# Kernel tuning notes

Hardware: AMD Instinct MI355X
Metric: run time of the kernel (lower is better)

The kernel has to match this reference:

```python
import jax, jax.numpy as jnp
import numpy as np
import math

NA, D, DA = 8, 512, 64
BSZ, THW = 4, 1024
EPS = 1e-5


def setup_inputs() -> dict:
    key = jax.random.key(0)
    ks = jax.random.split(key, 8)
    x = jax.random.normal(ks[0], (BSZ, THW, D), dtype=jnp.float32)
    B = jax.random.normal(ks[1], (NA, BSZ, THW, THW), dtype=jnp.float32)
    M = jax.random.randint(ks[2], (THW, THW), 0, 2, dtype=jnp.int32)
    # xavier-normal-ish params
    def xavier(k, shape, fan_in, fan_out):
        std = math.sqrt(2.0 / (fan_in + fan_out))
        return jax.random.normal(k, shape, dtype=jnp.float32) * std
    w_q = xavier(ks[3], (NA, D, DA), D, DA)
    w_k = xavier(ks[4], (NA, D, DA), D, DA)
    w_v = xavier(ks[5], (NA, D, DA), D, DA)
    w_proj = xavier(ks[6], (D, NA * DA), NA * DA, D)  # nn.Linear weight [out, in]
    gamma = jnp.ones((D,), dtype=jnp.float32)
    beta = jnp.zeros((D,), dtype=jnp.float32)
    return {"x": x, "B": B, "M": M, "gamma": gamma, "beta": beta,
            "w_q": w_q, "w_k": w_k, "w_v": w_v, "w_proj": w_proj}


def reference(x, B, M, gamma, beta, w_q, w_k, w_v, w_proj):
    b, thw, d = x.shape
    na, _, da = w_q.shape
    # pre-LayerNorm (residual is un-normalized x)
    mu = jnp.mean(x, axis=-1, keepdims=True)
    var = jnp.mean(jnp.square(x - mu), axis=-1, keepdims=True)
    xn = (x - mu) / jnp.sqrt(var + EPS) * gamma + beta  # [b, thw, d]
    # per-head QKV via shared projections: [na, b, thw, da]
    q = jnp.einsum('btd,hde->hbte', xn, w_q)
    k = jnp.einsum('btd,hde->hbte', xn, w_k)
    v = jnp.einsum('btd,hde->hbte', xn, w_v)
    temper = math.sqrt(da)
    attn = jnp.einsum('hbqe,hbke->hbqk', q, k) / temper + B  # [na, b, thw, thw]
    attn = jnp.where(M.astype(bool), jnp.float32(-10000.0), attn)
    p = jax.nn.softmax(attn, axis=-1)
    out = jnp.einsum('hbqk,hbke->hbqe', p, v)  # [na, b, thw, da]
    # concat heads on feature dim: [b, thw, na*da]
    out = out.transpose(1, 2, 0, 3).reshape(b, thw, na * da)
    out = out @ w_proj.T  # [b, thw, d]
    return out + x
```

## Files before the change

### kernel.cpp

```cpp
#include <hip/hip_runtime.h>

typedef __attribute__((ext_vector_type(4))) float f32x4;
typedef __attribute__((ext_vector_type(8))) short bf16x8;

#define AS1 __attribute__((address_space(1)))
#define AS3 __attribute__((address_space(3)))

static __device__ __forceinline__ void gl_lds16(const void* g, void* l) {
  __builtin_amdgcn_global_load_lds((const AS1 unsigned int*)g, (AS3 unsigned int*)l, 16, 0, 0);
}

static __device__ __forceinline__ unsigned short f2bf(float f) {
  union { float f; unsigned u; } v; v.f = f;
  unsigned r = v.u + 0x7FFFu + ((v.u >> 16) & 1u);
  return (unsigned short)(r >> 16);
}

__global__ __launch_bounds__(256) void prep_kernel(
    const float* __restrict__ wq, const float* __restrict__ wk,
    const float* __restrict__ wv, const float* __restrict__ wp,
    const int* __restrict__ M,
    unsigned short* __restrict__ Wt, unsigned short* __restrict__ Wp,
    unsigned* __restrict__ Mbits) {
  const int blk = blockIdx.x, tid = threadIdx.x;
  if (blk < 192) {
    __shared__ unsigned short t[64][72];
    const int which = blk >> 6, rem = blk & 63;
    const int h = rem >> 3, dt = rem & 7, d0 = dt * 64;
    const float* w = (which == 0) ? wq : ((which == 1) ? wk : wv);
    const float scale = (which == 0) ? 0.125f : 1.0f;
    const int r = tid >> 2, c4 = tid & 3;
    const float* src = w + h * 32768 + (d0 + r) * 64 + c4 * 16;
#pragma unroll
    for (int i = 0; i < 4; ++i) {
      float4 v = *(const float4*)(src + i * 4);
      t[c4 * 16 + i * 4 + 0][r] = f2bf(v.x * scale);
      t[c4 * 16 + i * 4 + 1][r] = f2bf(v.y * scale);
      t[c4 * 16 + i * 4 + 2][r] = f2bf(v.z * scale);
      t[c4 * 16 + i * 4 + 3][r] = f2bf(v.w * scale);
    }
    __syncthreads();
    const int e = tid >> 2;
    const int n = which * 512 + h * 64 + e;
    unsigned short* dst = Wt + (size_t)n * 512 + d0 + c4 * 16;
#pragma unroll
    for (int i = 0; i < 2; ++i) {
      bf16x8 o;
#pragma unroll
      for (int k = 0; k < 8; ++k) o[k] = (short)t[e][c4 * 16 + i * 8 + k];
      *(bf16x8*)(dst + i * 8) = o;
    }
  } else if (blk < 320) {
    const int base = ((blk - 192) * 256 + tid) * 8;
    float4 a = *(const float4*)(wp + base);
    float4 c = *(const float4*)(wp + base + 4);
    bf16x8 o;
    o[0] = (short)f2bf(a.x); o[1] = (short)f2bf(a.y);
    o[2] = (short)f2bf(a.z); o[3] = (short)f2bf(a.w);
    o[4] = (short)f2bf(c.x); o[5] = (short)f2bf(c.y);
    o[6] = (short)f2bf(c.z); o[7] = (short)f2bf(c.w);
    *(bf16x8*)(Wp + base) = o;
  } else {
    const int wi = (blk - 320) * 256 + tid;
    const int* row = M + wi * 32;
    unsigned bits = 0;
#pragma unroll
    for (int i = 0; i < 8; ++i) {
      int4 v = *(const int4*)(row + i * 4);
      bits |= (v.x != 0 ? 1u : 0u) << (i * 4 + 0);
      bits |= (v.y != 0 ? 1u : 0u) << (i * 4 + 1);
      bits |= (v.z != 0 ? 1u : 0u) << (i * 4 + 2);
      bits |= (v.w != 0 ? 1u : 0u) << (i * 4 + 3);
    }
    Mbits[wi] = bits;
  }
}


__global__ __launch_bounds__(256) void ln_kernel(
    const float* __restrict__ x, const float* __restrict__ gamma,
    const float* __restrict__ beta, unsigned short* __restrict__ xn) {
  const int wave = threadIdx.x >> 6, lane = threadIdx.x & 63;
  const int m = blockIdx.x * 4 + wave;
  const float* row = x + (size_t)m * 512;
  float4 a = *(const float4*)(row + lane * 8);
  float4 c = *(const float4*)(row + lane * 8 + 4);
  float s = a.x + a.y + a.z + a.w + c.x + c.y + c.z + c.w;
  float q = a.x * a.x + a.y * a.y + a.z * a.z + a.w * a.w +
            c.x * c.x + c.y * c.y + c.z * c.z + c.w * c.w;
#pragma unroll
  for (int off = 1; off < 64; off <<= 1) {
    s += __shfl_xor(s, off);
    q += __shfl_xor(q, off);
  }
  float mean = s * 0.001953125f;
  float var = q * 0.001953125f - mean * mean;
  float rstd = rsqrtf(var + 1e-5f);
  float4 g0 = *(const float4*)(gamma + lane * 8);
  float4 g1 = *(const float4*)(gamma + lane * 8 + 4);
  float4 b0 = *(const float4*)(beta + lane * 8);
  float4 b1 = *(const float4*)(beta + lane * 8 + 4);
  bf16x8 o;
  o[0] = (short)f2bf((a.x - mean) * rstd * g0.x + b0.x);
  o[1] = (short)f2bf((a.y - mean) * rstd * g0.y + b0.y);
  o[2] = (short)f2bf((a.z - mean) * rstd * g0.z + b0.z);
  o[3] = (short)f2bf((a.w - mean) * rstd * g0.w + b0.w);
  o[4] = (short)f2bf((c.x - mean) * rstd * g1.x + b1.x);
  o[5] = (short)f2bf((c.y - mean) * rstd * g1.y + b1.y);
  o[6] = (short)f2bf((c.z - mean) * rstd * g1.z + b1.z);
  o[7] = (short)f2bf((c.w - mean) * rstd * g1.w + b1.w);
  *(bf16x8*)(xn + (size_t)m * 512 + lane * 8) = o;
}

__global__ __launch_bounds__(256) void gemm_qkv(
    const unsigned short* __restrict__ A, const unsigned short* __restrict__ Bt,
    unsigned short* __restrict__ qout, unsigned short* __restrict__ kout,
    unsigned short* __restrict__ vout) {
  __shared__ __align__(16) unsigned short As[128 * 64];
  __shared__ __align__(16) unsigned short Bs[128 * 64];
  const int bx = blockIdx.x & 31, by = blockIdx.x >> 5;
  const int mbase = bx * 128, nbase = by * 128;
  const int tid = threadIdx.x;
  const int lane = tid & 63, wave = tid >> 6;
  const int lr = lane & 15, lg = lane >> 4;
  const int wm = wave >> 1, wn = wave & 1;
  f32x4 acc[4][4] = {};
  for (int kb = 0; kb < 8; ++kb) {
    const int kbase = kb * 64;
#pragma unroll
    for (int i = 0; i < 4; ++i) {
      int chunk = i * 256 + tid;
      int r = chunk >> 3, kc = chunk & 7;
      gl_lds16(A + (size_t)(mbase + r) * 512 + kbase + kc * 8, &As[chunk * 8]);
    }
#pragma unroll
    for (int i = 0; i < 4; ++i) {
      int chunk = i * 256 + tid;
      int r = chunk >> 3, kc = chunk & 7;
      gl_lds16(Bt + (size_t)(nbase + r) * 512 + kbase + kc * 8, &Bs[chunk * 8]);
    }
    __syncthreads();
#pragma unroll
    for (int ks = 0; ks < 2; ++ks) {
      bf16x8 af[4], bfr[4];
#pragma unroll
      for (int mi = 0; mi < 4; ++mi)
        af[mi] = *(const bf16x8*)&As[(wm * 64 + mi * 16 + lr) * 64 + ks * 32 + lg * 8];
#pragma unroll
      for (int ni = 0; ni < 4; ++ni)
        bfr[ni] = *(const bf16x8*)&Bs[(wn * 64 + ni * 16 + lr) * 64 + ks * 32 + lg * 8];
#pragma unroll
      for (int mi = 0; mi < 4; ++mi)
#pragma unroll
        for (int ni = 0; ni < 4; ++ni)
          acc[mi][ni] = __builtin_amdgcn_mfma_f32_16x16x32_bf16(af[mi], bfr[ni], acc[mi][ni], 0, 0, 0);
    }
    __syncthreads();
  }
#pragma unroll
  for (int ni = 0; ni < 4; ++ni) {
    const int n0 = nbase + wn * 64 + ni * 16;
    const int which = n0 >> 9, h = (n0 >> 6) & 7;
    const int e0 = (n0 & 63) + lr;
    unsigned short* dst = (which == 0) ? qout : ((which == 1) ? kout : vout);
    dst += (size_t)h * 262144 + e0;
#pragma unroll
    for (int mi = 0; mi < 4; ++mi) {
      const int m0 = mbase + wm * 64 + mi * 16 + lg * 4;
#pragma unroll
      for (int j = 0; j < 4; ++j) dst[(size_t)(m0 + j) * 64] = f2bf(acc[mi][ni][j]);
    }
  }
}

__global__ __launch_bounds__(256) void transpose_v(
    const unsigned short* __restrict__ vb, unsigned short* __restrict__ vt) {
  __shared__ unsigned short t[64][72];
  const int h = blockIdx.x >> 6, mt = blockIdx.x & 63;
  const unsigned short* src = vb + (size_t)h * 262144 + (size_t)mt * 64 * 64;
  const int tid = threadIdx.x;
#pragma unroll
  for (int i = 0; i < 2; ++i) {
    int c = tid + 256 * i;
    int r = c >> 3, c8 = c & 7;
    bf16x8 v = *(const bf16x8*)(src + r * 64 + c8 * 8);
#pragma unroll
    for (int k = 0; k < 8; ++k) t[c8 * 8 + k][r] = (unsigned short)v[k];
  }
  __syncthreads();
#pragma unroll
  for (int i = 0; i < 2; ++i) {
    int c = tid + 256 * i;
    int er = c >> 3, mc = c & 7;
    bf16x8 o;
#pragma unroll
    for (int k = 0; k < 8; ++k) o[k] = (short)t[er][mc * 8 + k];
    *(bf16x8*)(vt + (size_t)h * 262144 + (size_t)er * 4096 + mt * 64 + mc * 8) = o;
  }
}

__global__ __launch_bounds__(256, 2) void attn_kernel(
    const unsigned short* __restrict__ qb, const unsigned short* __restrict__ kbuf,
    const unsigned short* __restrict__ vt, const float* __restrict__ Bb,
    const unsigned* __restrict__ Mb, unsigned short* __restrict__ attno) {
  __shared__ __align__(16) unsigned short P[4][16 * 132];
  const int g = blockIdx.x;
  const int xcd = g & 7, slot = g >> 3;
  const int hb = xcd + 8 * (slot >> 4);
  const int qt = slot & 15;
  const int h = hb >> 2, b = hb & 3;
  const int lane = threadIdx.x & 63, wave = threadIdx.x >> 6;
  const int lr = lane & 15, lg = lane >> 4;
  const unsigned short* qh = qb + (size_t)h * 262144 + (size_t)b * 65536;
  const unsigned short* kh = kbuf + (size_t)h * 262144 + (size_t)b * 65536;
  const unsigned short* vh = vt + (size_t)h * 262144 + b * 1024;
  const int qa = qt * 64 + wave * 16 + lr;
  const bf16x8 qf0 = *(const bf16x8*)(qh + (size_t)qa * 64 + lg * 8);
  const bf16x8 qf1 = *(const bf16x8*)(qh + (size_t)qa * 64 + lg * 8 + 32);
  const int qc = qt * 64 + wave * 16 + lg * 4;
  const float* Bp = Bb + (size_t)hb * 1048576;
  float mrun[4] = {-1e30f, -1e30f, -1e30f, -1e30f};
  float lrun[4] = {0.f, 0.f, 0.f, 0.f};
  f32x4 of[4] = {};
  unsigned short* pw = &P[wave][0];
  for (int kv = 0; kv < 8; ++kv) {
    const int kvb = kv * 128;
    float bv[8][4];
    unsigned mwd[4][4];
#pragma unroll
    for (int j = 0; j < 4; ++j) {
      const float* brow = Bp + (size_t)(qc + j) * 1024 + kvb + lr;
#pragma unroll
      for (int f = 0; f < 8; ++f) bv[f][j] = brow[f * 16];
      uint4 mw = *(const uint4*)(Mb + (qc + j) * 32 + kv * 4);
      mwd[j][0] = mw.x; mwd[j][1] = mw.y; mwd[j][2] = mw.z; mwd[j][3] = mw.w;
    }
    bf16x8 kf0[8], kf1[8];
#pragma unroll
    for (int f = 0; f < 8; ++f) {
      const unsigned short* kp = kh + (size_t)(kvb + f * 16 + lr) * 64 + lg * 8;
      kf0[f] = *(const bf16x8*)kp;
      kf1[f] = *(const bf16x8*)(kp + 32);
    }
    f32x4 s[8];
#pragma unroll
    for (int f = 0; f < 8; ++f) {
      f32x4 c = {};
      c = __builtin_amdgcn_mfma_f32_16x16x32_bf16(qf0, kf0[f], c, 0, 0, 0);
      c = __builtin_amdgcn_mfma_f32_16x16x32_bf16(qf1, kf1[f], c, 0, 0, 0);
      s[f] = c;
    }
    float scl[4];
#pragma unroll
    for (int j = 0; j < 4; ++j) {
      float mm = -1e30f;
#pragma unroll
      for (int f = 0; f < 8; ++f) {
        float sv = s[f][j] + bv[f][j];
        if ((mwd[j][f >> 1] >> ((f & 1) * 16 + lr)) & 1u) sv = -10000.f;
        s[f][j] = sv;
        mm = fmaxf(mm, sv);
      }
      mm = fmaxf(mm, __shfl_xor(mm, 1));
      mm = fmaxf(mm, __shfl_xor(mm, 2));
      mm = fmaxf(mm, __shfl_xor(mm, 4));
      mm = fmaxf(mm, __shfl_xor(mm, 8));
      float mn = fmaxf(mrun[j], mm);
      scl[j] = __expf(mrun[j] - mn);
      mrun[j] = mn;
      float ps = 0.f;
#pragma unroll
      for (int f = 0; f < 8; ++f) {
        float p = __expf(s[f][j] - mn);
        s[f][j] = p;
        ps += p;
      }
      ps += __shfl_xor(ps, 1);
      ps += __shfl_xor(ps, 2);
      ps += __shfl_xor(ps, 4);
      ps += __shfl_xor(ps, 8);
      lrun[j] = lrun[j] * scl[j] + ps;
    }
#pragma unroll
    for (int e = 0; e < 4; ++e) {
      of[e][0] *= scl[0]; of[e][1] *= scl[1]; of[e][2] *= scl[2]; of[e][3] *= scl[3];
    }
#pragma unroll
    for (int f = 0; f < 8; ++f)
#pragma unroll
      for (int j = 0; j < 4; ++j)
        pw[(lg * 4 + j) * 132 + f * 16 + lr] = f2bf(s[f][j]);
    bf16x8 pa[4];
#pragma unroll
    for (int ks = 0; ks < 4; ++ks)
      pa[ks] = *(const bf16x8*)&pw[lr * 132 + ks * 32 + lg * 8];
    bf16x8 vf[4][4];
#pragma unroll
    for (int e = 0; e < 4; ++e) {
      const unsigned short* vp = vh + (size_t)(e * 16 + lr) * 4096 + kvb + lg * 8;
#pragma unroll
      for (int ks = 0; ks < 4; ++ks) vf[e][ks] = *(const bf16x8*)(vp + ks * 32);
    }
#pragma unroll
    for (int e = 0; e < 4; ++e)
#pragma unroll
      for (int ks = 0; ks < 4; ++ks)
        of[e] = __builtin_amdgcn_mfma_f32_16x16x32_bf16(pa[ks], vf[e][ks], of[e], 0, 0, 0);
  }
#pragma unroll
  for (int e = 0; e < 4; ++e)
#pragma unroll
    for (int j = 0; j < 4; ++j) {
      int m = b * 1024 + qc + j;
      attno[(size_t)h * 262144 + (size_t)m * 64 + e * 16 + lr] = f2bf(of[e][j] / lrun[j]);
    }
}

__global__ __launch_bounds__(256) void gemm_proj(
    const unsigned short* __restrict__ attno, const unsigned short* __restrict__ Wp,
    const float* __restrict__ x, float* __restrict__ out) {
  __shared__ __align__(16) unsigned short As[128 * 64];
  __shared__ __align__(16) unsigned short Bs[64 * 64];
  const int bx = blockIdx.x & 31, by = blockIdx.x >> 5;
  const int mbase = bx * 128, nbase = by * 64;
  const int tid = threadIdx.x;
  const int lane = tid & 63, wave = tid >> 6;
  const int lr = lane & 15, lg = lane >> 4;
  const int wm = wave >> 1, wn = wave & 1;
  f32x4 acc[4][2] = {};
  for (int kb = 0; kb < 8; ++kb) {
#pragma unroll
    for (int i = 0; i < 4; ++i) {
      int chunk = i * 256 + tid;
      int r = chunk >> 3, kc = chunk & 7;
      gl_lds16(attno + (size_t)kb * 262144 + (size_t)(mbase + r) * 64 + kc * 8, &As[chunk * 8]);
    }
#pragma unroll
    for (int i = 0; i < 2; ++i) {
      int chunk = i * 256 + tid;
      int r = chunk >> 3, kc = chunk & 7;
      gl_lds16(Wp + (size_t)(nbase + r) * 512 + kb * 64 + kc * 8, &Bs[chunk * 8]);
    }
    __syncthreads();
#pragma unroll
    for (int ks = 0; ks < 2; ++ks) {
      bf16x8 af[4], bfr[2];
#pragma unroll
      for (int mi = 0; mi < 4; ++mi)
        af[mi] = *(const bf16x8*)&As[(wm * 64 + mi * 16 + lr) * 64 + ks * 32 + lg * 8];
#pragma unroll
      for (int ni = 0; ni < 2; ++ni)
        bfr[ni] = *(const bf16x8*)&Bs[(wn * 32 + ni * 16 + lr) * 64 + ks * 32 + lg * 8];
#pragma unroll
      for (int mi = 0; mi < 4; ++mi)
#pragma unroll
        for (int ni = 0; ni < 2; ++ni)
          acc[mi][ni] = __builtin_amdgcn_mfma_f32_16x16x32_bf16(af[mi], bfr[ni], acc[mi][ni], 0, 0, 0);
    }
    __syncthreads();
  }
#pragma unroll
  for (int ni = 0; ni < 2; ++ni) {
    const int n = nbase + wn * 32 + ni * 16 + lr;
#pragma unroll
    for (int mi = 0; mi < 4; ++mi) {
      const int m0 = mbase + wm * 64 + mi * 16 + lg * 4;
#pragma unroll
      for (int j = 0; j < 4; ++j) {
        size_t idx = (size_t)(m0 + j) * 512 + n;
        out[idx] = acc[mi][ni][j] + x[idx];
      }
    }
  }
}

extern "C" void kernel_launch(void* const* d_in, const int* in_sizes, int n_in,
                              void* d_out, int out_size, void* d_ws, size_t ws_size,
                              hipStream_t stream) {
  const float* x = (const float*)d_in[0];
  const float* B = (const float*)d_in[1];
  const int* M = (const int*)d_in[2];
  const float* gamma = (const float*)d_in[3];
  const float* beta = (const float*)d_in[4];
  const float* wq = (const float*)d_in[5];
  const float* wk = (const float*)d_in[6];
  const float* wv = (const float*)d_in[7];
  const float* wp = (const float*)d_in[8];
  float* out = (float*)d_out;

  char* ws = (char*)d_ws;
  size_t o = 0;
  auto alloc = [&](size_t bytes) {
    void* p = ws + o;
    o += (bytes + 255) & ~(size_t)255;
    return p;
  };
  unsigned short* xn    = (unsigned short*)alloc(4096ull * 512 * 2);
  unsigned short* Wt    = (unsigned short*)alloc(1536ull * 512 * 2);
  unsigned short* Wp    = (unsigned short*)alloc(512ull * 512 * 2);
  unsigned*       Mb    = (unsigned*)alloc(1024ull * 32 * 4);
  unsigned short* qb    = (unsigned short*)alloc(8ull * 4096 * 64 * 2);
  unsigned short* kb    = (unsigned short*)alloc(8ull * 4096 * 64 * 2);
  unsigned short* vb    = (unsigned short*)alloc(8ull * 4096 * 64 * 2);
  unsigned short* vt    = (unsigned short*)alloc(8ull * 64 * 4096 * 2);
  unsigned short* attno = (unsigned short*)alloc(8ull * 4096 * 64 * 2);
  (void)ws_size; (void)in_sizes; (void)n_in; (void)out_size;

  hipLaunchKernelGGL(prep_kernel, dim3(448), dim3(256), 0, stream,
                     wq, wk, wv, wp, M, Wt, Wp, Mb);
  hipLaunchKernelGGL(ln_kernel, dim3(1024), dim3(256), 0, stream, x, gamma, beta, xn);
  hipLaunchKernelGGL(gemm_qkv, dim3(384), dim3(256), 0, stream, xn, Wt, qb, kb, vb);
  hipLaunchKernelGGL(transpose_v, dim3(512), dim3(256), 0, stream, vb, vt);
  hipLaunchKernelGGL(attn_kernel, dim3(512), dim3(256), 0, stream, qb, kb, vt, B, Mb, attno);
  hipLaunchKernelGGL(gemm_proj, dim3(256), dim3(256), 0, stream, attno, Wp, x, out);
}
```

Baseline: 293.5 us.

## Split attention over KV into four partitions with merge kernel; fuse LN into prep

The attention kernel becomes single-wave blocks, each handling 16 queries over one quarter of the key range. Each block writes unnormalized partial outputs plus running max and sum in fp32, and a new merge kernel combines the four partitions and writes bf16 output. This raises the grid from 512 to 8192 waves-blocks to improve latency hiding and occupancy on the memory-bound bias stream. The cost is extra fp32 partial traffic and one more launch. LayerNorm is also folded into the prep kernel to save a launch.

```diff
diff --git a/kernel.cpp b/kernel.cpp
--- a/kernel.cpp
+++ b/kernel.cpp
@@ -16,13 +16,47 @@
   return (unsigned short)(r >> 16);
 }
 
-__global__ __launch_bounds__(256) void prep_kernel(
+__global__ __launch_bounds__(256) void prepln_kernel(
     const float* __restrict__ wq, const float* __restrict__ wk,
     const float* __restrict__ wv, const float* __restrict__ wp,
-    const int* __restrict__ M,
+    const int* __restrict__ M, const float* __restrict__ x,
+    const float* __restrict__ gamma, const float* __restrict__ beta,
     unsigned short* __restrict__ Wt, unsigned short* __restrict__ Wp,
-    unsigned* __restrict__ Mbits) {
+    unsigned* __restrict__ Mbits, unsigned short* __restrict__ xn) {
   const int blk = blockIdx.x, tid = threadIdx.x;
+  if (blk >= 448) {
+    const int wave = tid >> 6, lane = tid & 63;
+    const int m = (blk - 448) * 4 + wave;
+    const float* row = x + (size_t)m * 512;
+    float4 a = *(const float4*)(row + lane * 8);
+    float4 c = *(const float4*)(row + lane * 8 + 4);
+    float s = a.x + a.y + a.z + a.w + c.x + c.y + c.z + c.w;
+    float q = a.x * a.x + a.y * a.y + a.z * a.z + a.w * a.w +
+              c.x * c.x + c.y * c.y + c.z * c.z + c.w * c.w;
+#pragma unroll
+    for (int off = 1; off < 64; off <<= 1) {
+      s += __shfl_xor(s, off);
+      q += __shfl_xor(q, off);
+    }
+    float mean = s * 0.001953125f;
+    float var = q * 0.001953125f - mean * mean;
+    float rstd = rsqrtf(var + 1e-5f);
+    float4 g0 = *(const float4*)(gamma + lane * 8);
+    float4 g1 = *(const float4*)(gamma + lane * 8 + 4);
+    float4 b0 = *(const float4*)(beta + lane * 8);
+    float4 b1 = *(const float4*)(beta + lane * 8 + 4);
+    bf16x8 o;
+    o[0] = (short)f2bf((a.x - mean) * rstd * g0.x + b0.x);
+    o[1] = (short)f2bf((a.y - mean) * rstd * g0.y + b0.y);
+    o[2] = (short)f2bf((a.z - mean) * rstd * g0.z + b0.z);
+    o[3] = (short)f2bf((a.w - mean) * rstd * g0.w + b0.w);
+    o[4] = (short)f2bf((c.x - mean) * rstd * g1.x + b1.x);
+    o[5] = (short)f2bf((c.y - mean) * rstd * g1.y + b1.y);
+    o[6] = (short)f2bf((c.z - mean) * rstd * g1.z + b1.z);
+    o[7] = (short)f2bf((c.w - mean) * rstd * g1.w + b1.w);
+    *(bf16x8*)(xn + (size_t)m * 512 + lane * 8) = o;
+    return;
+  }
   if (blk < 192) {
     __shared__ unsigned short t[64][72];
     const int which = blk >> 6, rem = blk & 63;
@@ -74,42 +108,6 @@
     }
     Mbits[wi] = bits;
   }
-}
-
-
-__global__ __launch_bounds__(256) void ln_kernel(
-    const float* __restrict__ x, const float* __restrict__ gamma,
-    const float* __restrict__ beta, unsigned short* __restrict__ xn) {
-  const int wave = threadIdx.x >> 6, lane = threadIdx.x & 63;
-  const int m = blockIdx.x * 4 + wave;
-  const float* row = x + (size_t)m * 512;
-  float4 a = *(const float4*)(row + lane * 8);
-  float4 c = *(const float4*)(row + lane * 8 + 4);
-  float s = a.x + a.y + a.z + a.w + c.x + c.y + c.z + c.w;
-  float q = a.x * a.x + a.y * a.y + a.z * a.z + a.w * a.w +
-            c.x * c.x + c.y * c.y + c.z * c.z + c.w * c.w;
-#pragma unroll
-  for (int off = 1; off < 64; off <<= 1) {
-    s += __shfl_xor(s, off);
-    q += __shfl_xor(q, off);
-  }
-  float mean = s * 0.001953125f;
-  float var = q * 0.001953125f - mean * mean;
-  float rstd = rsqrtf(var + 1e-5f);
-  float4 g0 = *(const float4*)(gamma + lane * 8);
-  float4 g1 = *(const float4*)(gamma + lane * 8 + 4);
-  float4 b0 = *(const float4*)(beta + lane * 8);
-  float4 b1 = *(const float4*)(beta + lane * 8 + 4);
-  bf16x8 o;
-  o[0] = (short)f2bf((a.x - mean) * rstd * g0.x + b0.x);
-  o[1] = (short)f2bf((a.y - mean) * rstd * g0.y + b0.y);
-  o[2] = (short)f2bf((a.z - mean) * rstd * g0.z + b0.z);
-  o[3] = (short)f2bf((a.w - mean) * rstd * g0.w + b0.w);
-  o[4] = (short)f2bf((c.x - mean) * rstd * g1.x + b1.x);
-  o[5] = (short)f2bf((c.y - mean) * rstd * g1.y + b1.y);
-  o[6] = (short)f2bf((c.z - mean) * rstd * g1.z + b1.z);
-  o[7] = (short)f2bf((c.w - mean) * rstd * g1.w + b1.w);
-  *(bf16x8*)(xn + (size_t)m * 512 + lane * 8) = o;
 }
 
 __global__ __launch_bounds__(256) void gemm_qkv(
@@ -199,32 +197,33 @@
   }
 }
 
-__global__ __launch_bounds__(256, 2) void attn_kernel(
+__global__ __launch_bounds__(64, 6) void attn_kernel(
     const unsigned short* __restrict__ qb, const unsigned short* __restrict__ kbuf,
     const unsigned short* __restrict__ vt, const float* __restrict__ Bb,
-    const unsigned* __restrict__ Mb, unsigned short* __restrict__ attno) {
-  __shared__ __align__(16) unsigned short P[4][16 * 132];
+    const unsigned* __restrict__ Mb, float* __restrict__ po,
+    float* __restrict__ pm, float* __restrict__ pl) {
+  __shared__ __align__(16) unsigned short P[16 * 132];
   const int g = blockIdx.x;
   const int xcd = g & 7, slot = g >> 3;
-  const int hb = xcd + 8 * (slot >> 4);
-  const int qt = slot & 15;
+  const int hb = xcd + 8 * (slot >> 8);
+  const int inner = slot & 255;
+  const int qt = inner >> 2, ks = inner & 3;
   const int h = hb >> 2, b = hb & 3;
-  const int lane = threadIdx.x & 63, wave = threadIdx.x >> 6;
+  const int lane = threadIdx.x;
   const int lr = lane & 15, lg = lane >> 4;
   const unsigned short* qh = qb + (size_t)h * 262144 + (size_t)b * 65536;
   const unsigned short* kh = kbuf + (size_t)h * 262144 + (size_t)b * 65536;
   const unsigned short* vh = vt + (size_t)h * 262144 + b * 1024;
-  const int qa = qt * 64 + wave * 16 + lr;
+  const int qa = qt * 16 + lr;
   const bf16x8 qf0 = *(const bf16x8*)(qh + (size_t)qa * 64 + lg * 8);
   const bf16x8 qf1 = *(const bf16x8*)(qh + (size_t)qa * 64 + lg * 8 + 32);
-  const int qc = qt * 64 + wave * 16 + lg * 4;
+  const int qc = qt * 16 + lg * 4;
   const float* Bp = Bb + (size_t)hb * 1048576;
   float mrun[4] = {-1e30f, -1e30f, -1e30f, -1e30f};
   float lrun[4] = {0.f, 0.f, 0.f, 0.f};
   f32x4 of[4] = {};
-  unsigned short* pw = &P[wave][0];
-  for (int kv = 0; kv < 8; ++kv) {
-    const int kvb = kv * 128;
+  for (int kv2 = 0; kv2 < 2; ++kv2) {
+    const int kvb = ks * 256 + kv2 * 128;
     float bv[8][4];
     unsigned mwd[4][4];
 #pragma unroll
@@ -232,7 +231,7 @@
       const float* brow = Bp + (size_t)(qc + j) * 1024 + kvb + lr;
 #pragma unroll
       for (int f = 0; f < 8; ++f) bv[f][j] = brow[f * 16];
-      uint4 mw = *(const uint4*)(Mb + (qc + j) * 32 + kv * 4);
+      uint4 mw = *(const uint4*)(Mb + (qc + j) * 32 + (kvb >> 5));
       mwd[j][0] = mw.x; mwd[j][1] = mw.y; mwd[j][2] = mw.z; mwd[j][3] = mw.w;
     }
     bf16x8 kf0[8], kf1[8];
@@ -289,31 +288,70 @@
     for (int f = 0; f < 8; ++f)
 #pragma unroll
       for (int j = 0; j < 4; ++j)
-        pw[(lg * 4 + j) * 132 + f * 16 + lr] = f2bf(s[f][j]);
+        P[(lg * 4 + j) * 132 + f * 16 + lr] = f2bf(s[f][j]);
     bf16x8 pa[4];
 #pragma unroll
-    for (int ks = 0; ks < 4; ++ks)
-      pa[ks] = *(const bf16x8*)&pw[lr * 132 + ks * 32 + lg * 8];
+    for (int k2 = 0; k2 < 4; ++k2)
+      pa[k2] = *(const bf16x8*)&P[lr * 132 + k2 * 32 + lg * 8];
     bf16x8 vf[4][4];
 #pragma unroll
     for (int e = 0; e < 4; ++e) {
       const unsigned short* vp = vh + (size_t)(e * 16 + lr) * 4096 + kvb + lg * 8;
 #pragma unroll
-      for (int ks = 0; ks < 4; ++ks) vf[e][ks] = *(const bf16x8*)(vp + ks * 32);
+      for (int k2 = 0; k2 < 4; ++k2) vf[e][k2] = *(const bf16x8*)(vp + k2 * 32);
     }
 #pragma unroll
     for (int e = 0; e < 4; ++e)
 #pragma unroll
-      for (int ks = 0; ks < 4; ++ks)
-        of[e] = __builtin_amdgcn_mfma_f32_16x16x32_bf16(pa[ks], vf[e][ks], of[e], 0, 0, 0);
-  }
+      for (int k2 = 0; k2 < 4; ++k2)
+        of[e] = __builtin_amdgcn_mfma_f32_16x16x32_bf16(pa[k2], vf[e][k2], of[e], 0, 0, 0);
+  }
+  const size_t prow = (size_t)ks * 32768 + hb * 1024 + qc;
 #pragma unroll
   for (int e = 0; e < 4; ++e)
 #pragma unroll
+    for (int j = 0; j < 4; ++j)
+      po[(prow + j) * 64 + e * 16 + lr] = of[e][j];
+  if (lr == 0) {
+#pragma unroll
     for (int j = 0; j < 4; ++j) {
-      int m = b * 1024 + qc + j;
-      attno[(size_t)h * 262144 + (size_t)m * 64 + e * 16 + lr] = f2bf(of[e][j] / lrun[j]);
-    }
+      pm[prow + j] = mrun[j];
+      pl[prow + j] = lrun[j];
+    }
+  }
+}
+
+__global__ __launch_bounds__(256) void merge_kernel(
+    const float* __restrict__ po, const float* __restrict__ pm,
+    const float* __restrict__ pl, unsigned short* __restrict__ attno) {
+  const int gt = blockIdx.x * 256 + threadIdx.x;
+  const int row = gt >> 2, c0 = (gt & 3) * 16;
+  float m0 = pm[row], m1 = pm[32768 + row], m2 = pm[65536 + row], m3 = pm[98304 + row];
+  float mx = fmaxf(fmaxf(m0, m1), fmaxf(m2, m3));
+  float w0 = __expf(m0 - mx), w1 = __expf(m1 - mx);
+  float w2 = __expf(m2 - mx), w3 = __expf(m3 - mx);
+  float l = w0 * pl[row] + w1 * pl[32768 + row] + w2 * pl[65536 + row] + w3 * pl[98304 + row];
+  float inv = 1.0f / l;
+  const size_t base = (size_t)row * 64 + c0;
+  f32x4 acc[4];
+#pragma unroll
+  for (int k = 0; k < 4; ++k) {
+    f32x4 a0 = *(const f32x4*)&po[base + k * 4];
+    f32x4 a1 = *(const f32x4*)&po[2097152 + base + k * 4];
+    f32x4 a2 = *(const f32x4*)&po[4194304 + base + k * 4];
+    f32x4 a3 = *(const f32x4*)&po[6291456 + base + k * 4];
+    acc[k] = w0 * a0 + w1 * a1 + w2 * a2 + w3 * a3;
+  }
+  bf16x8 o0, o1;
+#pragma unroll
+  for (int i = 0; i < 4; ++i) {
+    o0[i] = (short)f2bf(acc[0][i] * inv);
+    o0[4 + i] = (short)f2bf(acc[1][i] * inv);
+    o1[i] = (short)f2bf(acc[2][i] * inv);
+    o1[4 + i] = (short)f2bf(acc[3][i] * inv);
+  }
+  *(bf16x8*)(attno + base) = o0;
+  *(bf16x8*)(attno + base + 8) = o1;
 }
 
 __global__ __launch_bounds__(256) void gemm_proj(
@@ -404,13 +442,16 @@
   unsigned short* vb    = (unsigned short*)alloc(8ull * 4096 * 64 * 2);
   unsigned short* vt    = (unsigned short*)alloc(8ull * 64 * 4096 * 2);
   unsigned short* attno = (unsigned short*)alloc(8ull * 4096 * 64 * 2);
+  float*          po    = (float*)alloc(4ull * 32768 * 64 * 4);
+  float*          pm    = (float*)alloc(4ull * 32768 * 4);
+  float*          pl    = (float*)alloc(4ull * 32768 * 4);
   (void)ws_size; (void)in_sizes; (void)n_in; (void)out_size;
 
-  hipLaunchKernelGGL(prep_kernel, dim3(448), dim3(256), 0, stream,
-                     wq, wk, wv, wp, M, Wt, Wp, Mb);
-  hipLaunchKernelGGL(ln_kernel, dim3(1024), dim3(256), 0, stream, x, gamma, beta, xn);
+  hipLaunchKernelGGL(prepln_kernel, dim3(1472), dim3(256), 0, stream,
+                     wq, wk, wv, wp, M, x, gamma, beta, Wt, Wp, Mb, xn);
   hipLaunchKernelGGL(gemm_qkv, dim3(384), dim3(256), 0, stream, xn, Wt, qb, kb, vb);
   hipLaunchKernelGGL(transpose_v, dim3(512), dim3(256), 0, stream, vb, vt);
-  hipLaunchKernelGGL(attn_kernel, dim3(512), dim3(256), 0, stream, qb, kb, vt, B, Mb, attno);
+  hipLaunchKernelGGL(attn_kernel, dim3(8192), dim3(64), 0, stream, qb, kb, vt, B, Mb, po, pm, pl);
+  hipLaunchKernelGGL(merge_kernel, dim3(512), dim3(256), 0, stream, po, pm, pl, attno);
   hipLaunchKernelGGL(gemm_proj, dim3(256), dim3(256), 0, stream, attno, Wp, x, out);
 }
```

Result: slower. 400.6 us (+36.5%).
